# Kernel optimization log

Hardware: AMD Instinct MI355X
Metric: run time of the kernel (lower is better)

The kernel has to match this reference:

```python
import jax, jax.numpy as jnp
import numpy as np
from jax import lax

OUT_SIZE = 224  # original input spatial size (output_size of anomaly map)
NUM_NEIGHBORS = 9
SIGMA = 4.0
KSIZE = 2 * int(4.0 * SIGMA + 0.5) + 1  # 33, kornia-style kernel size


def avg_pool3(x):
    # AvgPool2d(3, 1, 1), count_include_pad=True -> sum over 3x3 window / 9
    s = lax.reduce_window(x, 0.0, lax.add, (1, 1, 3, 3), (1, 1, 1, 1),
                          [(0, 0), (0, 0), (1, 1), (1, 1)])
    return s / 9.0


def euclidean_dist(x, y):
    # x: [..., N, E], y: [..., M, E] -> [..., N, M]
    x_norm = jnp.sum(x * x, axis=-1, keepdims=True)
    y_norm = jnp.sum(y * y, axis=-1, keepdims=True)
    res = x_norm - 2.0 * jnp.matmul(x, jnp.swapaxes(y, -2, -1)) + jnp.swapaxes(y_norm, -2, -1)
    return jnp.sqrt(jnp.clip(res, 0.0))


def gaussian_blur(x):
    # x: [B,1,H,W]; separable Gaussian, reflect padding (kornia GaussianBlur2d default)
    r = KSIZE // 2
    t = jnp.arange(KSIZE, dtype=x.dtype) - r
    k = jnp.exp(-(t * t) / (2.0 * SIGMA * SIGMA))
    k = k / jnp.sum(k)
    xp = jnp.pad(x, ((0, 0), (0, 0), (r, r), (r, r)), mode='reflect')
    kh = k.reshape(1, 1, KSIZE, 1)
    kw = k.reshape(1, 1, 1, KSIZE)
    y = lax.conv_general_dilated(xp, kh, (1, 1), 'VALID',
                                 dimension_numbers=('NCHW', 'OIHW', 'NCHW'))
    return lax.conv_general_dilated(y, kw, (1, 1), 'VALID',
                                    dimension_numbers=('NCHW', 'OIHW', 'NCHW'))


def compute_anomaly_score(patch_scores, locations, embedding, memory_bank):
    # patch_scores/locations: [B, P]; embedding: [B*P, E]; memory_bank: [M, E]
    batch, num_patches = patch_scores.shape
    bidx = jnp.arange(batch)
    max_patches = jnp.argmax(patch_scores, axis=1)                       # [B]
    max_feats = embedding.reshape(batch, num_patches, -1)[bidx, max_patches]  # [B,E]
    score = patch_scores[bidx, max_patches]                              # [B]
    nn_index = locations[bidx, max_patches]                              # [B]
    nn_sample = memory_bank[nn_index]                                    # [B,E]
    n_nb = min(NUM_NEIGHBORS, memory_bank.shape[0])
    d_bank = euclidean_dist(nn_sample, memory_bank)                      # [B,M]
    _, support = lax.top_k(-d_bank, n_nb)                                # [B,k] smallest
    sup_feats = memory_bank[support]                                     # [B,k,E]
    d = euclidean_dist(max_feats[:, None, :], sup_feats)[:, 0, :]        # [B,k]
    weights = (1.0 - jax.nn.softmax(d, axis=1))[:, 0]                    # [B]
    return weights * score


def setup_inputs() -> dict:
    key = jax.random.key(0)
    k1, k2, k3 = jax.random.split(key, 3)
    feat2 = jax.random.normal(k1, (8, 512, 28, 28), dtype=jnp.float32)
    feat3 = jax.random.normal(k2, (8, 1024, 14, 14), dtype=jnp.float32)
    memory_bank = jax.random.normal(k3, (20000, 1536), dtype=jnp.float32)
    return {'feat2': feat2, 'feat3': feat3, 'memory_bank': memory_bank}


def reference(feat2, feat3, memory_bank):
    # feature pooling (AvgPool2d(3,1,1) on each backbone layer)
    f2 = avg_pool3(feat2)
    f3 = avg_pool3(feat3)
    batch, _, height, width = f2.shape
    # generate_embedding: bilinear upsample deeper layer, concat along channels
    f3u = jax.image.resize(f3, (batch, f3.shape[1], height, width), method='bilinear')
    emb = jnp.concatenate([f2, f3u], axis=1)                 # [B,1536,28,28]
    emb_dim = emb.shape[1]
    embedding = emb.transpose(0, 2, 3, 1).reshape(-1, emb_dim)  # [B*784, 1536]
    # nearest_neighbors with n_neighbors=1
    dist = euclidean_dist(embedding, memory_bank)            # [N, M]
    patch_scores = jnp.min(dist, axis=1)
    locations = jnp.argmin(dist, axis=1)
    patch_scores = patch_scores.reshape(batch, -1)
    locations = locations.reshape(batch, -1)
    pred_score = compute_anomaly_score(patch_scores, locations, embedding, memory_bank)
    # anomaly map: bilinear upsample patch scores to input size + gaussian blur
    score_map = patch_scores.reshape(batch, 1, width, height)
    amap = jax.image.resize(score_map, (batch, 1, OUT_SIZE, OUT_SIZE), method='bilinear')
    anomaly_map = gaussian_blur(amap)
    return anomaly_map, pred_score
```

## Files before the change

kernel.cpp:

```cpp
#include <hip/hip_runtime.h>
#include <math.h>

#define NB 8
#define C2 512
#define C3 1024
#define H2 28
#define W2 28
#define H3 14
#define W3 14
#define EDIM 1536
#define PPB (H2*W2)
#define NPATCH (NB*PPB)
#define MPAD 6400
#define MBANK 20000
#define OUTW 224
#define NNB 9
#define KS 33
#define KR 16
#define NMT 25
#define NNTB 157
#define CHUNKS 8
#define CH (MBANK/CHUNKS)
#define MPB 64
#define NSLAB 24

#define SXQ 63.5f
#define SYQ (127.0f/6.0f)

typedef __attribute__((ext_vector_type(4))) int   i32x4;

#define LEXLT(va,ia,vb,ib) ((va) < (vb) || ((va)==(vb) && (ia)<(ib)))
#define CSWAP(va,ia,vb,ib) { if (LEXLT(va,ia,vb,ib)) { float _tv=(vb); int _ti=(ib); (vb)=(va); (ib)=(ia); (va)=_tv; (ia)=_ti; } }

#define BAR() asm volatile("s_barrier" ::: "memory")
#define WAITV0() asm volatile("s_waitcnt vmcnt(0)" ::: "memory")

__device__ __forceinline__ void gload16(const void* g, void* l) {
  __builtin_amdgcn_global_load_lds(
      (const __attribute__((address_space(1))) unsigned int*)g,
      (__attribute__((address_space(3))) unsigned int*)l, 16, 0, 0);
}
__device__ __forceinline__ signed char q8(float x, float s) {
  int v = (int)rintf(x * s);
  v = v > 127 ? 127 : (v < -127 ? -127 : v);
  return (signed char)v;
}


__global__ __launch_bounds__(256) void pool2_kernel(const float* __restrict__ in,
    float* __restrict__ emb32, signed char* __restrict__ embq) {
  int bid = blockIdx.x;
  int cg = bid & 7; int h = (bid >> 3) % H2; int b = bid / (8*H2);
  int t = threadIdx.x;
  __shared__ float s3[3][64][29];
  for (int li = t; li < 3*64*28; li += 256) {
    int w = li % 28; int c = (li/28) & 63; int dh = li/(28*64);
    int hh = h + dh - 1;
    float v = 0.f;
    if (hh >= 0 && hh < H2) v = in[((size_t)(b*C2) + cg*64 + c)*784 + hh*28 + w];
    s3[dh][c][w] = v;
  }
  __syncthreads();
  for (int o = t; o < 64*28; o += 256) {
    int c = o & 63, w = o >> 6;
    float s = 0.f;
    #pragma unroll
    for (int dh = 0; dh < 3; ++dh) {
      s += s3[dh][c][w];
      if (w > 0)  s += s3[dh][c][w-1];
      if (w < 27) s += s3[dh][c][w+1];
    }
    s *= (1.f/9.f);
    size_t idx = ((size_t)(b*PPB) + h*28 + w)*EDIM + cg*64 + c;
    emb32[idx] = s;
    embq[idx] = q8(s, SXQ);
  }
}

__global__ void pool3_kernel(const float* __restrict__ in, float* __restrict__ f3p) {
  int id = blockIdx.x*blockDim.x + threadIdx.x;
  if (id >= NB*C3*H3*W3) return;
  int w = id % W3, h = (id / W3) % H3, c = (id / (H3*W3)) % C3, b = id / (C3*H3*W3);
  const float* src = in + (size_t)(b*C3 + c)*H3*W3;
  float s = 0.f;
  #pragma unroll
  for (int dh=-1; dh<=1; ++dh) {
    int hh = h+dh; if (hh<0||hh>=H3) continue;
    #pragma unroll
    for (int dw=-1; dw<=1; ++dw) {
      int ww = w+dw; if (ww<0||ww>=W3) continue;
      s += src[hh*W3+ww];
    }
  }
  f3p[(size_t)id] = s * (1.f/9.f);
}

__global__ __launch_bounds__(256) void up3_kernel(const float* __restrict__ f3p,
    float* __restrict__ emb32, signed char* __restrict__ embq) {
  int bid = blockIdx.x;
  int cg = bid & 15; int i = (bid >> 4) % H2; int b = bid / (16*H2);
  int t = threadIdx.x;
  float sy = i*0.5f - 0.25f; sy = fminf(fmaxf(sy,0.f),(float)(H3-1));
  int y0 = (int)sy; int y1 = min(y0+1,H3-1); float fy = sy - (float)y0;
  __shared__ float r2[2][64][15];
  for (int li = t; li < 2*64*14; li += 256) {
    int w = li % 14; int c = (li/14) & 63; int yy = li/(14*64);
    int ysrc = yy ? y1 : y0;
    r2[yy][c][w] = f3p[((size_t)(b*C3) + cg*64 + c)*196 + ysrc*14 + w];
  }
  __syncthreads();
  for (int o = t; o < 64*28; o += 256) {
    int c = o & 63, j = o >> 6;
    float sx = j*0.5f - 0.25f; sx = fminf(fmaxf(sx,0.f),(float)(W3-1));
    int x0 = (int)sx; int x1 = min(x0+1,W3-1); float fx = sx - (float)x0;
    float v = (1.f-fy)*((1.f-fx)*r2[0][c][x0] + fx*r2[0][c][x1])
            +      fy *((1.f-fx)*r2[1][c][x0] + fx*r2[1][c][x1]);
    size_t idx = ((size_t)(b*PPB) + i*28 + j)*EDIM + C2 + cg*64 + c;
    emb32[idx] = v;
    embq[idx] = q8(v, SXQ);
  }
}


__global__ void bank_prep_kernel(const float* __restrict__ bank, signed char* __restrict__ bankq,
                                 float* __restrict__ yn) {
  int w = (blockIdx.x*blockDim.x + threadIdx.x) >> 6;
  int lane = threadIdx.x & 63;
  if (w >= MBANK) return;
  const float4* p = reinterpret_cast<const float4*>(bank + (size_t)w*EDIM);
  int* q = reinterpret_cast<int*>(bankq + (size_t)w*EDIM);
  float acc = 0.f;
  #pragma unroll
  for (int k = 0; k < EDIM/4/64; ++k) {
    int k4 = lane + k*64;
    float4 v = p[k4];
    acc = fmaf(v.x,v.x,acc); acc = fmaf(v.y,v.y,acc);
    acc = fmaf(v.z,v.z,acc); acc = fmaf(v.w,v.w,acc);
    unsigned pk = ((unsigned)(unsigned char)q8(v.x, SYQ))
                | ((unsigned)(unsigned char)q8(v.y, SYQ) << 8)
                | ((unsigned)(unsigned char)q8(v.z, SYQ) << 16)
                | ((unsigned)(unsigned char)q8(v.w, SYQ) << 24);
    q[k4] = (int)pk;
  }
  #pragma unroll
  for (int s = 32; s; s >>= 1) acc += __shfl_xor(acc, s);
  if (lane == 0) yn[w] = acc;
}


__global__ __launch_bounds__(512, 4) void dist_min_i8(
    const signed char* __restrict__ A, const signed char* __restrict__ B,
    const float* __restrict__ yn, float* __restrict__ outq, int* __restrict__ outi)
{
  __shared__ __align__(16) unsigned char LDSC[49152];
  const int t = threadIdx.x;
  const int lane = t & 63, wid = t >> 6;
  const int wr = wid >> 1, wc = wid & 1;

  const int nwg = NMT*NNTB;
  int orig = blockIdx.x;
  int xcd = orig & 7, loc = orig >> 3;
  int qq = nwg >> 3, rm = nwg & 7;
  int wg = (xcd < rm ? xcd*(qq+1) : rm*(qq+1) + (xcd-rm)*qq) + loc;
  const int mt = wg / NNTB, nt = wg % NNTB;
  const int m0 = mt*256, n0 = nt*128;

  const int l3 = lane >> 3, l7 = lane & 7;
  const int D = l7 ^ l3;
  const int koS = (D & 3) << 4;
  const int rhi = D >> 2;
  const int rA0 = wid*32 + (l3<<1) + rhi;
  const int rA1 = rA0 + 16;
  const int rB  = wid*16 + (l3<<1) + rhi;
  const char* Ac = (const char*)A + (size_t)m0*EDIM;
  const char* Bc = (const char*)B;
  const unsigned aoff0 = (unsigned)(rA0*EDIM + koS);
  const unsigned aoff1 = (unsigned)(rA1*EDIM + koS);
  int bn = n0 + rB; bn = bn < MBANK ? bn : MBANK-1;
  const unsigned boff = (unsigned)bn*(unsigned)EDIM + (unsigned)koS;
  char* const aDst = (char*)LDSC + wid*2048;
  char* const bDst = (char*)LDSC + 16384 + wid*1024;

  const int h = lane & 15, g = lane >> 4;
  const int csw = (((h & 1) << 2) | g) ^ (h >> 1);
  const unsigned abyte = (unsigned)(wr*4096 + (h>>1)*128 + csw*16);
  const unsigned bbyte = (unsigned)(16384 + wc*4096 + (h>>1)*128 + csw*16);

  i32x4 acc[4][4];
  #pragma unroll
  for (int i = 0; i < 4; ++i)
    #pragma unroll
    for (int j = 0; j < 4; ++j) acc[i][j] = (i32x4){0,0,0,0};

  gload16(Ac + aoff0, aDst);
  gload16(Ac + aoff1, aDst + 1024);
  gload16(Bc + boff,  bDst);
  WAITV0();
  BAR();

  #pragma unroll 2
  for (int p = 0; p < NSLAB; ++p) {
    const unsigned sb = (unsigned)(p & 1)*24576u;
    if (p < NSLAB-1) {
      const unsigned sw = (unsigned)((p+1) & 1)*24576u;
      gload16(Ac + aoff0 + (p+1)*64, aDst + sw);
      gload16(Ac + aoff1 + (p+1)*64, aDst + sw + 1024);
      gload16(Bc + boff  + (p+1)*64, bDst + sw);
    }
    i32x4 af[4], bfv[4];
    #pragma unroll
    for (int j = 0; j < 4; ++j)
      bfv[j] = *(const i32x4*)(LDSC + sb + bbyte + j*1024);
    #pragma unroll
    for (int i = 0; i < 4; ++i)
      af[i] = *(const i32x4*)(LDSC + sb + abyte + i*1024);
    __builtin_amdgcn_s_setprio(1);
    #pragma unroll
    for (int i = 0; i < 4; ++i)
      #pragma unroll
      for (int j = 0; j < 4; ++j)
        acc[i][j] = __builtin_amdgcn_mfma_i32_16x16x64_i8(af[i], bfv[j], acc[i][j], 0, 0, 0);
    __builtin_amdgcn_s_setprio(0);
    WAITV0();
    BAR();
  }

  const float NEG2INV = -2.0f * (2.0f/127.0f) * (6.0f/127.0f);
  float ynv[4];
  #pragma unroll
  for (int j = 0; j < 4; ++j) {
    int col = n0 + wc*64 + j*16 + h;
    ynv[j] = col < MBANK ? yn[col] : INFINITY;
  }
  float* smin = (float*)LDSC;
  int* sidx = (int*)(LDSC + 2048);
  #pragma unroll
  for (int i = 0; i < 4; ++i) {
    #pragma unroll
    for (int r = 0; r < 4; ++r) {
      float v = INFINITY; int ix = 0x7fffffff;
      #pragma unroll
      for (int j = 0; j < 4; ++j) {
        float q = fmaf(NEG2INV, (float)acc[i][j][r], ynv[j]);
        int col = n0 + wc*64 + j*16 + h;
        if (q < v || (q == v && col < ix)) { v = q; ix = col; }
      }
      #pragma unroll
      for (int m = 1; m < 16; m <<= 1) {
        float ov = __shfl_xor(v, m);
        int   oi = __shfl_xor(ix, m);
        if (ov < v || (ov == v && oi < ix)) { v = ov; ix = oi; }
      }
      if (h == 0) {
        int rl = wr*64 + i*16 + g*4 + r;
        smin[rl*2 + wc] = v;
        sidx[rl*2 + wc] = ix;
      }
    }
  }
  __syncthreads();
  if (t < 256) {
    float v0 = smin[t*2], v1 = smin[t*2+1];
    int   i0 = sidx[t*2], i1 = sidx[t*2+1];
    float v; int ix;
    if (LEXLT(v1, i1, v0, i0)) { v = v1; ix = i1; } else { v = v0; ix = i0; }
    int row = m0 + t;
    if (row < NPATCH) {
      outq[(size_t)nt*NPATCH + row] = v;
      outi[(size_t)nt*NPATCH + row] = ix;
    }
  }
}

__global__ void reduce_min_kernel(const float* __restrict__ outq, const int* __restrict__ outi,
                                  int* __restrict__ loc) {
  int r = blockIdx.x*blockDim.x + threadIdx.x;
  if (r >= NPATCH) return;
  float bv = INFINITY; int bi = 0x7fffffff;
  for (int s = 0; s < NNTB; ++s) {
    float v = outq[(size_t)s*NPATCH + r];
    int  ix = outi[(size_t)s*NPATCH + r];
    if (v < bv || (v == bv && ix < bi)) { bv = v; bi = ix; }
  }
  loc[r] = bi;
}

__global__ void rescore_kernel(const float* __restrict__ emb32, const float* __restrict__ bank,
                               const float* __restrict__ yn,
                               const int* __restrict__ loc, float* __restrict__ ps) {
  int w = (blockIdx.x*blockDim.x + threadIdx.x) >> 6;
  int lane = threadIdx.x & 63;
  if (w >= NPATCH) return;
  int j = loc[w];
  const float4* x = reinterpret_cast<const float4*>(emb32 + (size_t)w*EDIM);
  const float4* y = reinterpret_cast<const float4*>(bank + (size_t)j*EDIM);
  float accd = 0.f, accx = 0.f;
  #pragma unroll
  for (int k = 0; k < EDIM/4/64; ++k) {
    float4 a = x[lane + k*64], b = y[lane + k*64];
    accd = fmaf(a.x,b.x,accd); accd = fmaf(a.y,b.y,accd);
    accd = fmaf(a.z,b.z,accd); accd = fmaf(a.w,b.w,accd);
    accx = fmaf(a.x,a.x,accx); accx = fmaf(a.y,a.y,accx);
    accx = fmaf(a.z,a.z,accx); accx = fmaf(a.w,a.w,accx);
  }
  #pragma unroll
  for (int s = 32; s; s >>= 1) { accd += __shfl_xor(accd, s); accx += __shfl_xor(accx, s); }
  if (lane == 0) ps[w] = sqrtf(fmaxf(accx - 2.f*accd + yn[j], 0.f));
}


__global__ void argmax_kernel(const float* __restrict__ ps, const int* __restrict__ loc,
                              float* __restrict__ bscore, int* __restrict__ brow, int* __restrict__ bnn) {
  __shared__ float sv[256]; __shared__ int si[256];
  int b = blockIdx.x, t = threadIdx.x;
  float bv = -INFINITY; int bi = 0x7fffffff;
  for (int p = t; p < PPB; p += 256) {
    float v = ps[b*PPB + p];
    if (v > bv || (v == bv && p < bi)) { bv = v; bi = p; }
  }
  sv[t] = bv; si[t] = bi; __syncthreads();
  for (int s = 128; s; s >>= 1) {
    if (t < s) {
      if (sv[t+s] > sv[t] || (sv[t+s] == sv[t] && si[t+s] < si[t])) { sv[t] = sv[t+s]; si[t] = si[t+s]; }
    }
    __syncthreads();
  }
  if (t == 0) {
    bscore[b] = sv[0];
    brow[b]   = b*PPB + si[0];
    bnn[b]    = loc[b*PPB + si[0]];
  }
}

__global__ __launch_bounds__(256) void dbank_kernel(
    const float* __restrict__ bank, const float* __restrict__ yn,
    const int* __restrict__ bnn, float* __restrict__ dbank)
{
  __shared__ float xs[8][EDIM];
  int t = threadIdx.x;
  for (int idx = t*4; idx < 8*EDIM; idx += 256*4) {
    int b = idx / EDIM, k = idx % EDIM;
    float4 v = *reinterpret_cast<const float4*>(bank + (size_t)bnn[b]*EDIM + k);
    *reinterpret_cast<float4*>(&xs[b][k]) = v;
  }
  __syncthreads();
  int lane = t & 63, w = t >> 6;
  for (int u = 0; u < MPB/4; ++u) {
    int m = blockIdx.x*MPB + u*4 + w;
    if (m < MBANK) {
      const float4* yp = reinterpret_cast<const float4*>(bank + (size_t)m*EDIM);
      float acc[8] = {0.f,0.f,0.f,0.f,0.f,0.f,0.f,0.f};
      for (int k4 = lane; k4 < EDIM/4; k4 += 64) {
        float4 y = yp[k4];
        int k = k4*4;
        #pragma unroll
        for (int b = 0; b < 8; ++b) {
          acc[b] = fmaf(y.x, xs[b][k+0], acc[b]);
          acc[b] = fmaf(y.y, xs[b][k+1], acc[b]);
          acc[b] = fmaf(y.z, xs[b][k+2], acc[b]);
          acc[b] = fmaf(y.w, xs[b][k+3], acc[b]);
        }
      }
      #pragma unroll
      for (int b = 0; b < 8; ++b) {
        float a = acc[b];
        #pragma unroll
        for (int s = 32; s; s >>= 1) a += __shfl_xor(a, s);
        acc[b] = a;
      }
      if (lane == 0) {
        #pragma unroll
        for (int b = 0; b < 8; ++b) {
          int nn = bnn[b];
          float d2 = yn[nn] - 2.f*acc[b] + yn[m];
          dbank[(size_t)b*MBANK + m] = sqrtf(fmaxf(d2, 0.f));
        }
      }
    }
  }
}


__global__ __launch_bounds__(256) void top9_stage1(const float* __restrict__ dbank,
                                                   float* __restrict__ cv, int* __restrict__ ci) {
  int b = blockIdx.x / CHUNKS, ch = blockIdx.x % CHUNKS;
  const float* db = dbank + (size_t)b*MBANK + ch*CH;
  int t = threadIdx.x;

  float v0=INFINITY,v1=INFINITY,v2=INFINITY,v3=INFINITY,v4=INFINITY,
        v5=INFINITY,v6=INFINITY,v7=INFINITY,v8=INFINITY;
  int i0=0x7fffffff,i1=0x7fffffff,i2=0x7fffffff,i3=0x7fffffff,i4=0x7fffffff,
      i5=0x7fffffff,i6=0x7fffffff,i7=0x7fffffff,i8=0x7fffffff;

  for (int s = 0; s < (CH+255)/256; ++s) {
    int m = t + s*256;
    if (m < CH) {
      float nv = db[m]; int ni = ch*CH + m;
      if (LEXLT(nv,ni,v8,i8)) {
        v8 = nv; i8 = ni;
        CSWAP(v8,i8,v7,i7); CSWAP(v7,i7,v6,i6); CSWAP(v6,i6,v5,i5); CSWAP(v5,i5,v4,i4);
        CSWAP(v4,i4,v3,i3); CSWAP(v3,i3,v2,i2); CSWAP(v2,i2,v1,i1); CSWAP(v1,i1,v0,i0);
      }
    }
  }

  __shared__ float sv[256*9];
  __shared__ int   si[256*9];
  __shared__ float rv[256]; __shared__ int ri[256]; __shared__ int rp[256];
  sv[t*9+0]=v0; sv[t*9+1]=v1; sv[t*9+2]=v2; sv[t*9+3]=v3; sv[t*9+4]=v4;
  sv[t*9+5]=v5; sv[t*9+6]=v6; sv[t*9+7]=v7; sv[t*9+8]=v8;
  si[t*9+0]=i0; si[t*9+1]=i1; si[t*9+2]=i2; si[t*9+3]=i3; si[t*9+4]=i4;
  si[t*9+5]=i5; si[t*9+6]=i6; si[t*9+7]=i7; si[t*9+8]=i8;
  __syncthreads();

  for (int r = 0; r < NNB; ++r) {
    float bv = INFINITY; int bix = 0x7fffffff; int bp = -1;
    #pragma unroll
    for (int u = 0; u < 9; ++u) {
      float v = sv[t*9+u]; int ix = si[t*9+u];
      if (LEXLT(v,ix,bv,bix)) { bv = v; bix = ix; bp = t*9+u; }
    }
    rv[t] = bv; ri[t] = bix; rp[t] = bp; __syncthreads();
    for (int s = 128; s; s >>= 1) {
      if (t < s) {
        if (LEXLT(rv[t+s],ri[t+s],rv[t],ri[t])) { rv[t]=rv[t+s]; ri[t]=ri[t+s]; rp[t]=rp[t+s]; }
      }
      __syncthreads();
    }
    if (t == 0) {
      cv[blockIdx.x*NNB + r] = rv[0];
      ci[blockIdx.x*NNB + r] = ri[0];
      sv[rp[0]] = INFINITY; si[rp[0]] = 0x7fffffff;
    }
    __syncthreads();
  }
}


__global__ __launch_bounds__(128) void finalize_kernel(
    const float* __restrict__ cv, const int* __restrict__ ci,
    const float* __restrict__ emb32, const float* __restrict__ bank,
    const float* __restrict__ yn, const int* __restrict__ brow,
    const float* __restrict__ bscore, float* __restrict__ out) {
  __shared__ float sv[128]; __shared__ int si[128];
  __shared__ float wv[128]; __shared__ int wi[128]; __shared__ int wp[128];
  __shared__ int supp[NNB]; __shared__ float ds[NNB];
  int b = blockIdx.x, t = threadIdx.x;
  if (t < CHUNKS*NNB) { sv[t] = cv[b*CHUNKS*NNB + t]; si[t] = ci[b*CHUNKS*NNB + t]; }
  else { sv[t] = INFINITY; si[t] = 0x7fffffff; }
  __syncthreads();
  for (int r = 0; r < NNB; ++r) {
    wv[t] = sv[t]; wi[t] = si[t]; wp[t] = t; __syncthreads();
    for (int s = 64; s; s >>= 1) {
      if (t < s) {
        if (LEXLT(wv[t+s],wi[t+s],wv[t],wi[t])) { wv[t]=wv[t+s]; wi[t]=wi[t+s]; wp[t]=wp[t+s]; }
      }
      __syncthreads();
    }
    if (t == 0) {
      supp[r] = wi[0];
      sv[wp[0]] = INFINITY; si[wp[0]] = 0x7fffffff;
    }
    __syncthreads();
  }
  int lane = t & 63, w = t >> 6;
  int row = brow[b];
  const float* x = emb32 + (size_t)row*EDIM;
  for (int j = w; j < NNB; j += 2) {
    const float* y = bank + (size_t)supp[j]*EDIM;
    float accd = 0.f, accx = 0.f;
    for (int k = lane; k < EDIM; k += 64) {
      float a = x[k];
      accd = fmaf(a, y[k], accd);
      accx = fmaf(a, a, accx);
    }
    #pragma unroll
    for (int s = 32; s; s >>= 1) { accd += __shfl_xor(accd, s); accx += __shfl_xor(accx, s); }
    if (lane == 0) ds[j] = sqrtf(fmaxf(accx - 2.f*accd + yn[supp[j]], 0.f));
  }
  __syncthreads();
  if (t == 0) {
    float mx = -INFINITY;
    #pragma unroll
    for (int j = 0; j < NNB; ++j) mx = fmaxf(mx, ds[j]);
    float s = 0.f;
    #pragma unroll
    for (int j = 0; j < NNB; ++j) s += expf(ds[j] - mx);
    float wgt = 1.f - expf(ds[0] - mx) / s;
    out[b] = wgt * bscore[b];
  }
}


__device__ __forceinline__ int refl224(int x) {
  if (x < 0) return -x;
  if (x > OUTW-1) return 2*(OUTW-1) - x;
  return x;
}

__global__ __launch_bounds__(256) void upblurh_kernel(const float* __restrict__ ps,
                                                      float* __restrict__ tmp) {
  int b = blockIdx.x / OUTW, i = blockIdx.x % OUTW;
  int t = threadIdx.x;
  __shared__ float l[W2];
  __shared__ float graw[KS];
  if (t < KS) {
    float x = (float)t - (float)KR;
    graw[t] = expf(-(x*x) / (2.f*4.f*4.f));
  }
  float sy = ((float)i + 0.5f)*0.125f - 0.5f; sy = fminf(fmaxf(sy,0.f),(float)(H2-1));
  int y0 = (int)sy; int y1 = min(y0+1,H2-1); float fy = sy - (float)y0;
  if (t < W2) {
    const float* p = ps + b*PPB;
    l[t] = (1.f-fy)*p[y0*W2+t] + fy*p[y1*W2+t];
  }
  __syncthreads();
  if (t >= OUTW) return;
  float gsum = 0.f;
  #pragma unroll
  for (int u = 0; u < KS; ++u) gsum += graw[u];
  float winv = 1.f / gsum;
  float s = 0.f;
  #pragma unroll
  for (int v = 0; v < KS; ++v) {
    int jj = refl224(t - KR + v);
    float sx = ((float)jj + 0.5f)*0.125f - 0.5f; sx = fminf(fmaxf(sx,0.f),(float)(W2-1));
    int x0 = (int)sx; int x1 = min(x0+1,W2-1); float fx = sx - (float)x0;
    s = fmaf(graw[v]*winv, (1.f-fx)*l[x0] + fx*l[x1], s);
  }
  tmp[((size_t)b*OUTW + i)*OUTW + t] = s;
}

__global__ __launch_bounds__(256) void blurv_kernel(const float* __restrict__ in,
                                                    float* __restrict__ out) {
  __shared__ float graw[KS];
  int t = threadIdx.x;
  if (t < KS) {
    float x = (float)t - (float)KR;
    graw[t] = expf(-(x*x) / (2.f*4.f*4.f));
  }
  __syncthreads();
  int id = blockIdx.x*blockDim.x + t;
  if (id >= NB*OUTW*OUTW) return;
  float gsum = 0.f;
  #pragma unroll
  for (int u = 0; u < KS; ++u) gsum += graw[u];
  float winv = 1.f / gsum;
  int j = id % OUTW, i = (id/OUTW) % OUTW, b = id/(OUTW*OUTW);
  float s = 0.f;
  #pragma unroll
  for (int u = 0; u < KS; ++u) {
    int ii = refl224(i - KR + u);
    s = fmaf(graw[u]*winv, in[((size_t)b*OUTW + ii)*OUTW + j], s);
  }
  out[id] = s;
}


extern "C" void kernel_launch(void* const* d_in, const int* in_sizes, int n_in,
                              void* d_out, int out_size, void* d_ws, size_t ws_size,
                              hipStream_t stream) {
  const float* feat2 = (const float*)d_in[0];
  const float* feat3 = (const float*)d_in[1];
  const float* bank  = (const float*)d_in[2];
  float* out = (float*)d_out;

  char* base = (char*)d_ws;
  size_t off = 0;
  auto alloc = [&](size_t nbytes) -> char* {
    char* p = base + off;
    off += ((nbytes + 255) & ~(size_t)255);
    return p;
  };
  float*       emb32 = (float*)      alloc((size_t)NPATCH*EDIM*4);
  signed char* embq  = (signed char*)alloc((size_t)MPAD*EDIM);
  signed char* bankq = (signed char*)alloc((size_t)MBANK*EDIM);
  float* f3p    = (float*)alloc((size_t)NB*C3*H3*W3*4);
  float* yn     = (float*)alloc(MBANK*4);
  float* outq   = (float*)alloc((size_t)NNTB*NPATCH*4);
  int*   outi   = (int*)  alloc((size_t)NNTB*NPATCH*4);
  float* ps     = (float*)alloc(NPATCH*4);
  int*   loc    = (int*)  alloc(NPATCH*4);
  float* bscore = (float*)alloc(NB*4);
  int*   brow   = (int*)  alloc(NB*4);
  int*   bnn    = (int*)  alloc(NB*4);
  float* dbank  = (float*)alloc((size_t)NB*MBANK*4);
  float* cv     = (float*)alloc(NB*CHUNKS*NNB*4);
  int*   ci     = (int*)  alloc(NB*CHUNKS*NNB*4);
  float* tmp    = (float*)alloc((size_t)NB*OUTW*OUTW*4);

  pool2_kernel<<<NB*H2*8, 256, 0, stream>>>(feat2, emb32, embq);
  {
    int n = NB*C3*H3*W3;
    pool3_kernel<<<(n+255)/256, 256, 0, stream>>>(feat3, f3p);
  }
  up3_kernel<<<NB*H2*16, 256, 0, stream>>>(f3p, emb32, embq);
  bank_prep_kernel<<<(MBANK*64)/256, 256, 0, stream>>>(bank, bankq, yn);

  dist_min_i8<<<NMT*NNTB, 512, 0, stream>>>(embq, bankq, yn, outq, outi);
  reduce_min_kernel<<<(NPATCH+255)/256, 256, 0, stream>>>(outq, outi, loc);
  rescore_kernel<<<(NPATCH*64)/256, 256, 0, stream>>>(emb32, bank, yn, loc, ps);

  argmax_kernel<<<NB, 256, 0, stream>>>(ps, loc, bscore, brow, bnn);
  dbank_kernel<<<(MBANK+MPB-1)/MPB, 256, 0, stream>>>(bank, yn, bnn, dbank);
  top9_stage1<<<NB*CHUNKS, 256, 0, stream>>>(dbank, cv, ci);
  finalize_kernel<<<NB, 128, 0, stream>>>(cv, ci, emb32, bank, yn, brow, bscore,
                                          out + NB*OUTW*OUTW);

  {
    upblurh_kernel<<<NB*OUTW, 256, 0, stream>>>(ps, tmp);
    int n = NB*OUTW*OUTW;
    blurv_kernel<<<(n+255)/256, 256, 0, stream>>>(tmp, out);
  }
}
```

Measured before the change: 542.6 us.

## Triple-buffer int8 distance GEMM loads and fuse min-reduce into rescore

The int8 distance kernel now keeps three LDS stages instead of two and prefetches two slabs ahead, waiting with vmcnt(3) so one slab's loads stay in flight during compute. This is meant to hide global-to-LDS latency, at the cost of raising LDS from 48KB to 72KB per block. At 72KB per block the four blocks per CU requested by the launch bounds probably no longer fit, so occupancy may drop. Separately, the per-row reduction over column tiles is folded into the rescore kernel, using a wave-wide shuffle reduce. This removes one launch and the round trip of loc through memory.

```diff
diff --git a/kernel.cpp b/kernel.cpp
--- a/kernel.cpp
+++ b/kernel.cpp
@@ -33,6 +33,7 @@
 #define CSWAP(va,ia,vb,ib) { if (LEXLT(va,ia,vb,ib)) { float _tv=(vb); int _ti=(ib); (vb)=(va); (ib)=(ia); (va)=_tv; (ia)=_ti; } }
 
 #define BAR() asm volatile("s_barrier" ::: "memory")
+#define WAITV3() asm volatile("s_waitcnt vmcnt(3)" ::: "memory")
 #define WAITV0() asm volatile("s_waitcnt vmcnt(0)" ::: "memory")
 
 __device__ __forceinline__ void gload16(const void* g, void* l) {
@@ -152,7 +153,7 @@
     const signed char* __restrict__ A, const signed char* __restrict__ B,
     const float* __restrict__ yn, float* __restrict__ outq, int* __restrict__ outi)
 {
-  __shared__ __align__(16) unsigned char LDSC[49152];
+  __shared__ __align__(16) unsigned char LDSC[73728];
   const int t = threadIdx.x;
   const int lane = t & 63, wid = t >> 6;
   const int wr = wid >> 1, wc = wid & 1;
@@ -195,17 +196,20 @@
   gload16(Ac + aoff0, aDst);
   gload16(Ac + aoff1, aDst + 1024);
   gload16(Bc + boff,  bDst);
-  WAITV0();
+  gload16(Ac + aoff0 + 64, aDst + 24576);
+  gload16(Ac + aoff1 + 64, aDst + 24576 + 1024);
+  gload16(Bc + boff  + 64, bDst + 24576);
+  WAITV3();
   BAR();
 
-  #pragma unroll 2
+  #pragma unroll 3
   for (int p = 0; p < NSLAB; ++p) {
-    const unsigned sb = (unsigned)(p & 1)*24576u;
-    if (p < NSLAB-1) {
-      const unsigned sw = (unsigned)((p+1) & 1)*24576u;
-      gload16(Ac + aoff0 + (p+1)*64, aDst + sw);
-      gload16(Ac + aoff1 + (p+1)*64, aDst + sw + 1024);
-      gload16(Bc + boff  + (p+1)*64, bDst + sw);
+    const unsigned sb = (unsigned)(p % 3)*24576u;
+    if (p < NSLAB-2) {
+      const unsigned sw = (unsigned)((p+2) % 3)*24576u;
+      gload16(Ac + aoff0 + (p+2)*64, aDst + sw);
+      gload16(Ac + aoff1 + (p+2)*64, aDst + sw + 1024);
+      gload16(Bc + boff  + (p+2)*64, bDst + sw);
     }
     i32x4 af[4], bfv[4];
     #pragma unroll
@@ -221,7 +225,7 @@
       for (int j = 0; j < 4; ++j)
         acc[i][j] = __builtin_amdgcn_mfma_i32_16x16x64_i8(af[i], bfv[j], acc[i][j], 0, 0, 0);
     __builtin_amdgcn_s_setprio(0);
-    WAITV0();
+    if (p < NSLAB-2) { WAITV3(); } else { WAITV0(); }
     BAR();
   }
 
@@ -272,26 +276,28 @@
   }
 }
 
-__global__ void reduce_min_kernel(const float* __restrict__ outq, const int* __restrict__ outi,
-                                  int* __restrict__ loc) {
-  int r = blockIdx.x*blockDim.x + threadIdx.x;
-  if (r >= NPATCH) return;
-  float bv = INFINITY; int bi = 0x7fffffff;
-  for (int s = 0; s < NNTB; ++s) {
-    float v = outq[(size_t)s*NPATCH + r];
-    int  ix = outi[(size_t)s*NPATCH + r];
-    if (v < bv || (v == bv && ix < bi)) { bv = v; bi = ix; }
-  }
-  loc[r] = bi;
-}
-
-__global__ void rescore_kernel(const float* __restrict__ emb32, const float* __restrict__ bank,
-                               const float* __restrict__ yn,
-                               const int* __restrict__ loc, float* __restrict__ ps) {
+
+__global__ __launch_bounds__(256) void minrescore_kernel(
+    const float* __restrict__ outq, const int* __restrict__ outi,
+    const float* __restrict__ emb32, const float* __restrict__ bank,
+    const float* __restrict__ yn, int* __restrict__ loc, float* __restrict__ ps) {
   int w = (blockIdx.x*blockDim.x + threadIdx.x) >> 6;
   int lane = threadIdx.x & 63;
   if (w >= NPATCH) return;
-  int j = loc[w];
+  float bv = INFINITY; int bi = 0x7fffffff;
+  for (int s = lane; s < NNTB; s += 64) {
+    float v = outq[(size_t)s*NPATCH + w];
+    int  ix = outi[(size_t)s*NPATCH + w];
+    if (LEXLT(v, ix, bv, bi)) { bv = v; bi = ix; }
+  }
+  #pragma unroll
+  for (int m = 32; m; m >>= 1) {
+    float ov = __shfl_xor(bv, m);
+    int   oi = __shfl_xor(bi, m);
+    if (LEXLT(ov, oi, bv, bi)) { bv = ov; bi = oi; }
+  }
+  int j = bi;
+  if (lane == 0) loc[w] = j;
   const float4* x = reinterpret_cast<const float4*>(emb32 + (size_t)w*EDIM);
   const float4* y = reinterpret_cast<const float4*>(bank + (size_t)j*EDIM);
   float accd = 0.f, accx = 0.f;
@@ -598,8 +604,7 @@
   bank_prep_kernel<<<(MBANK*64)/256, 256, 0, stream>>>(bank, bankq, yn);
 
   dist_min_i8<<<NMT*NNTB, 512, 0, stream>>>(embq, bankq, yn, outq, outi);
-  reduce_min_kernel<<<(NPATCH+255)/256, 256, 0, stream>>>(outq, outi, loc);
-  rescore_kernel<<<(NPATCH*64)/256, 256, 0, stream>>>(emb32, bank, yn, loc, ps);
+  minrescore_kernel<<<(NPATCH*64)/256, 256, 0, stream>>>(outq, outi, emb32, bank, yn, loc, ps);
 
   argmax_kernel<<<NB, 256, 0, stream>>>(ps, loc, bscore, brow, bnn);
   dbank_kernel<<<(MBANK+MPB-1)/MPB, 256, 0, stream>>>(bank, yn, bnn, dbank);
```

After: 505.6 us. -6.8%, faster.
